# Kernel optimization log

Measured on AMD Instinct MI355X. Metric: run time of the kernel, lower is better.

The kernel has to match this reference:

```python
import jax, jax.numpy as jnp
import numpy as np

S, B, D, H, F = 1024, 8, 1024, 16, 4096
HD = D // H
EPS = 1e-5


def setup_inputs() -> dict:
    key = jax.random.key(0)
    ks = jax.random.split(key, 12)
    sc_d = 1.0 / np.sqrt(D)
    sc_f = 1.0 / np.sqrt(F)
    return {
        "src": jax.random.normal(ks[0], (S, B, D), jnp.float32),
        "in_proj_w": jax.random.uniform(ks[1], (3 * D, D), jnp.float32, -sc_d, sc_d),
        "in_proj_b": jnp.zeros((3 * D,), jnp.float32),
        "out_w": jax.random.uniform(ks[2], (D, D), jnp.float32, -sc_d, sc_d),
        "out_b": jnp.zeros((D,), jnp.float32),
        "w1": jax.random.uniform(ks[3], (F, D), jnp.float32, -sc_d, sc_d),
        "b1": jax.random.uniform(ks[4], (F,), jnp.float32, -sc_d, sc_d),
        "w2": jax.random.uniform(ks[5], (D, F), jnp.float32, -sc_f, sc_f),
        "b2": jax.random.uniform(ks[6], (D,), jnp.float32, -sc_f, sc_f),
        "g1": jnp.ones((D,), jnp.float32),
        "be1": jnp.zeros((D,), jnp.float32),
        "g2": jnp.ones((D,), jnp.float32),
        "be2": jnp.zeros((D,), jnp.float32),
    }


def _layer_norm(x, g, b):
    mu = jnp.mean(x, axis=-1, keepdims=True)
    var = jnp.mean(jnp.square(x - mu), axis=-1, keepdims=True)
    return (x - mu) * jax.lax.rsqrt(var + EPS) * g + b


def reference(src, in_proj_w, in_proj_b, out_w, out_b, w1, b1, w2, b2, g1, be1, g2, be2):
    wq, wk, wv = jnp.split(in_proj_w, 3, axis=0)
    bq, bk, bv = jnp.split(in_proj_b, 3, axis=0)
    scale = 1.0 / np.sqrt(HD)
    # src: [S, B, D] -> q/k/v: [S, B, H, HD]
    q = (src @ wq.T + bq).reshape(S, B, H, HD) * scale
    k = (src @ wk.T + bk).reshape(S, B, H, HD)
    v = (src @ wv.T + bv).reshape(S, B, H, HD)
    # full score matrix [B, H, S, S] (matches the unfused bmm/softmax/bmm)
    scores = jnp.einsum("sbhd,tbhd->bhst", q, k)
    attn = jax.nn.softmax(scores, axis=-1)
    ctx = jnp.einsum("bhst,tbhd->sbhd", attn, v).reshape(S, B, D)
    attn_out = ctx @ out_w.T + out_b
    x = _layer_norm(src + attn_out, g1, be1)
    ffn = jax.nn.relu(x @ w1.T + b1) @ w2.T + b2
    return _layer_norm(x + ffn, g2, be2)
```

## Files before the change

kernel.cpp:

```cpp
#include <hip/hip_runtime.h>
#include <hip/hip_bf16.h>
#include <stdint.h>

typedef __bf16 bf16x8 __attribute__((ext_vector_type(8)));
typedef __bf16 bf16x4 __attribute__((ext_vector_type(4)));
typedef float floatx4 __attribute__((ext_vector_type(4)));

typedef __attribute__((address_space(1))) void gvoid;
typedef __attribute__((address_space(3))) void lvoid;

__device__ __forceinline__ void async_load16(const __bf16* g, __bf16* l) {
  __builtin_amdgcn_global_load_lds((gvoid*)g, (lvoid*)l, 16, 0, 0);
}

__device__ __forceinline__ bf16x8 ld8(const float* p) {
  const floatx4 a = *(const floatx4*)p;
  const floatx4 b = *(const floatx4*)(p + 4);
  bf16x8 r;
  r[0] = (__bf16)a[0]; r[1] = (__bf16)a[1];
  r[2] = (__bf16)a[2]; r[3] = (__bf16)a[3];
  r[4] = (__bf16)b[0]; r[5] = (__bf16)b[1];
  r[6] = (__bf16)b[2]; r[7] = (__bf16)b[3];
  return r;
}

__global__ __launch_bounds__(256) void cvt_kernel(const float* __restrict__ in,
                                                  __bf16* __restrict__ out,
                                                  int n) {
  const int i = (blockIdx.x * 256 + threadIdx.x) * 8;
  if (i < n) *(bf16x8*)(out + i) = ld8(in + i);
}

constexpr int BM = 128, BN = 128, BK = 32;

template <typename AT, typename BT, int EPI>
__global__ __launch_bounds__(256, 2) void gemm_bt(
    const AT* __restrict__ A, const BT* __restrict__ Bt,
    const float* __restrict__ bias, const float* __restrict__ resf,
    const __bf16* __restrict__ resb, __bf16* __restrict__ o0,
    __bf16* __restrict__ o2, int M, int N, int K, int ldb) {
  constexpr bool AF = sizeof(AT) == 4;
  constexpr bool BF = sizeof(BT) == 4;
  __shared__ __align__(16) __bf16 As[BM * BK];
  __shared__ __align__(16) __bf16 Bs[BN * BK];
  const int tid = threadIdx.x;
  const int w = tid >> 6;
  const int lane = tid & 63;
  const int l16 = lane & 15;
  const int quad = lane >> 4;
  const int wm = (w & 1) * 64;
  const int wn = (w >> 1) * 64;
  const int bm = blockIdx.y * BM;
  const int bn = blockIdx.x * BN;

  floatx4 acc[4][4];
#pragma unroll
  for (int i = 0; i < 4; ++i)
#pragma unroll
    for (int j = 0; j < 4; ++j) acc[i][j] = (floatx4){0.f, 0.f, 0.f, 0.f};

  const int srow = tid >> 2, scol = (tid & 3) * 8;
  const int arow = lane >> 2, acol = (lane & 3) * 8;
  const AT* Ag;
  if constexpr (AF) Ag = A + (int64_t)(bm + srow) * K + scol;
  else Ag = A + (int64_t)(bm + w * 32 + arow) * K + acol;
  const BT* Bg;
  if constexpr (BF) Bg = Bt + (int64_t)(bn + srow) * ldb + scol;
  else Bg = Bt + (int64_t)(bn + w * 32 + arow) * ldb + acol;
  __bf16* AsW = As + (w * 32) * BK;
  __bf16* BsW = Bs + (w * 32) * BK;

  bf16x8 a0, a1, b0, b1;
  if constexpr (AF) {
    a0 = ld8(Ag);
    a1 = ld8(Ag + (int64_t)64 * K);
  }
  if constexpr (BF) {
    b0 = ld8(Bg);
    b1 = ld8(Bg + (int64_t)64 * ldb);
  }

  for (int k0 = 0; k0 < K; k0 += BK) {
    __syncthreads();
    if constexpr (AF) {
      *(bf16x8*)(As + tid * 8) = a0;
      *(bf16x8*)(As + 2048 + tid * 8) = a1;
    } else {
      async_load16(Ag + k0, AsW);
      async_load16(Ag + k0 + 16 * K, AsW + 16 * BK);
    }
    if constexpr (BF) {
      *(bf16x8*)(Bs + tid * 8) = b0;
      *(bf16x8*)(Bs + 2048 + tid * 8) = b1;
    } else {
      async_load16(Bg + k0, BsW);
      async_load16(Bg + k0 + 16 * ldb, BsW + 16 * BK);
    }
    __syncthreads();
    if constexpr (AF) {
      if (k0 + BK < K) {
        a0 = ld8(Ag + k0 + BK);
        a1 = ld8(Ag + k0 + BK + (int64_t)64 * K);
      }
    }
    if constexpr (BF) {
      if (k0 + BK < K) {
        b0 = ld8(Bg + k0 + BK);
        b1 = ld8(Bg + k0 + BK + (int64_t)64 * ldb);
      }
    }
    bf16x8 af[4], bfr[4];
#pragma unroll
    for (int i = 0; i < 4; ++i) {
      af[i] = *(const bf16x8*)(As + (wm + i * 16 + l16) * BK + quad * 8);
      bfr[i] = *(const bf16x8*)(Bs + (wn + i * 16 + l16) * BK + quad * 8);
    }
#pragma unroll
    for (int mi = 0; mi < 4; ++mi)
#pragma unroll
      for (int ni = 0; ni < 4; ++ni)
        acc[mi][ni] = __builtin_amdgcn_mfma_f32_16x16x32_bf16(
            af[mi], bfr[ni], acc[mi][ni], 0, 0, 0);
  }

#pragma unroll
  for (int ni = 0; ni < 4; ++ni) {
    const int gn = bn + wn + ni * 16 + l16;
    const float bv = (EPI == 3) ? 0.f : bias[gn];
#pragma unroll
    for (int mi = 0; mi < 4; ++mi) {
#pragma unroll
      for (int r = 0; r < 4; ++r) {
        const int gm = bm + wm + mi * 16 + quad * 4 + r;
        float v = acc[mi][ni][r] + bv;
        if (EPI == 0) {
          if (gn < 2048) {
            o0[(int64_t)gm * 2048 + gn] = (__bf16)(gn < 1024 ? v * 0.125f : v);
          } else {
            const int nn = gn - 2048, hh = nn >> 6, d = nn & 63;
            const int s = gm >> 3, b = gm & 7;
            o2[((b * 16 + hh) * 64 + d) * 1024 + s] = (__bf16)v;
          }
        } else {
          if (EPI == 1) v += resf[(int64_t)gm * N + gn];
          if (EPI == 3 || EPI == 4) v += (float)resb[(int64_t)gm * N + gn];
          if (EPI == 2) v = fmaxf(v, 0.f);
          o0[(int64_t)gm * N + gn] = (__bf16)v;
        }
      }
    }
  }
}

__global__ __launch_bounds__(256) void attn_flash(
    const __bf16* __restrict__ qk, const __bf16* __restrict__ vT,
    __bf16* __restrict__ ctx) {
  constexpr int S = 1024, PSTR = 36;
  constexpr int ROWSTR = 8 * 2048;
  __shared__ __align__(16) __bf16 Kb[2][2048];
  __shared__ __align__(16) __bf16 Vb[2][2048];
  __shared__ __align__(16) __bf16 Pt[4][32 * PSTR];
  const int tid = threadIdx.x;
  const int w = tid >> 6;
  const int lane = tid & 63;
  const int l16 = lane & 15;
  const int quad = lane >> 4;
  const int bh = blockIdx.y, bidx = bh >> 4, h = bh & 15;
  const int qbase = blockIdx.x * 128 + w * 32;

  const __bf16* qp =
      qk + ((int64_t)(qbase + l16) * 8 + bidx) * 2048 + h * 64 + quad * 8;
  bf16x8 aq[2][2];
  aq[0][0] = *(const bf16x8*)qp;
  aq[0][1] = *(const bf16x8*)(qp + 32);
  aq[1][0] = *(const bf16x8*)(qp + 16 * ROWSTR);
  aq[1][1] = *(const bf16x8*)(qp + 16 * ROWSTR + 32);

  const __bf16* kg = qk + 1024 +
      ((int64_t)((w >> 1) * 16 + l16) * 8 + bidx) * 2048 + h * 64 +
      ((w & 1) * 4 + quad) * 8;
  const __bf16* vg =
      vT + ((int64_t)bh * 64 + w * 16 + l16) * 1024 + quad * 8;
  __bf16* pt = Pt[w];

  floatx4 o[2][4];
  float la[2][4];
#pragma unroll
  for (int rt = 0; rt < 2; ++rt)
#pragma unroll
    for (int j = 0; j < 4; ++j) {
      o[rt][j] = (floatx4){0.f, 0.f, 0.f, 0.f};
      la[rt][j] = 0.f;
    }

  async_load16(kg, Kb[0] + w * 512);
  async_load16(vg, Vb[0] + w * 512);
  int cur = 0;

  for (int t0 = 0; t0 < S; t0 += 32) {
    __syncthreads();
    if (t0 + 32 < S) {
      async_load16(kg + (int64_t)(t0 + 32) * ROWSTR, Kb[cur ^ 1] + w * 512);
      async_load16(vg + (t0 + 32), Vb[cur ^ 1] + w * 512);
    }

    bf16x8 kf[4], vv[4];
#pragma unroll
    for (int f = 0; f < 4; ++f) {
      kf[f] = *(const bf16x8*)(Kb[cur] + f * 512 + lane * 8);
      vv[f] = *(const bf16x8*)(Vb[cur] + f * 512 + lane * 8);
    }

    floatx4 s00 = (floatx4){0.f, 0.f, 0.f, 0.f};
    floatx4 s01 = (floatx4){0.f, 0.f, 0.f, 0.f};
    floatx4 s10 = (floatx4){0.f, 0.f, 0.f, 0.f};
    floatx4 s11 = (floatx4){0.f, 0.f, 0.f, 0.f};
    s00 = __builtin_amdgcn_mfma_f32_16x16x32_bf16(aq[0][0], kf[0], s00, 0, 0, 0);
    s00 = __builtin_amdgcn_mfma_f32_16x16x32_bf16(aq[0][1], kf[1], s00, 0, 0, 0);
    s01 = __builtin_amdgcn_mfma_f32_16x16x32_bf16(aq[0][0], kf[2], s01, 0, 0, 0);
    s01 = __builtin_amdgcn_mfma_f32_16x16x32_bf16(aq[0][1], kf[3], s01, 0, 0, 0);
    s10 = __builtin_amdgcn_mfma_f32_16x16x32_bf16(aq[1][0], kf[0], s10, 0, 0, 0);
    s10 = __builtin_amdgcn_mfma_f32_16x16x32_bf16(aq[1][1], kf[1], s10, 0, 0, 0);
    s11 = __builtin_amdgcn_mfma_f32_16x16x32_bf16(aq[1][0], kf[2], s11, 0, 0, 0);
    s11 = __builtin_amdgcn_mfma_f32_16x16x32_bf16(aq[1][1], kf[3], s11, 0, 0, 0);

#pragma unroll
    for (int r = 0; r < 4; ++r) {
      const int row0 = (quad * 4 + r) * PSTR;
      const float p00 = __expf(s00[r]);
      const float p01 = __expf(s01[r]);
      la[0][r] += p00 + p01;
      pt[row0 + l16] = (__bf16)p00;
      pt[row0 + 16 + l16] = (__bf16)p01;
      const int row1 = (16 + quad * 4 + r) * PSTR;
      const float p10 = __expf(s10[r]);
      const float p11 = __expf(s11[r]);
      la[1][r] += p10 + p11;
      pt[row1 + l16] = (__bf16)p10;
      pt[row1 + 16 + l16] = (__bf16)p11;
    }
    const bf16x8 pa0 = *(const bf16x8*)(pt + l16 * PSTR + quad * 8);
    const bf16x8 pa1 = *(const bf16x8*)(pt + (16 + l16) * PSTR + quad * 8);
#pragma unroll
    for (int j = 0; j < 4; ++j) {
      o[0][j] = __builtin_amdgcn_mfma_f32_16x16x32_bf16(pa0, vv[j], o[0][j], 0, 0, 0);
      o[1][j] = __builtin_amdgcn_mfma_f32_16x16x32_bf16(pa1, vv[j], o[1][j], 0, 0, 0);
    }
    cur ^= 1;
  }

#pragma unroll
  for (int rt = 0; rt < 2; ++rt)
#pragma unroll
    for (int r = 0; r < 4; ++r) {
      float s = la[rt][r];
      s += __shfl_xor(s, 1, 64);
      s += __shfl_xor(s, 2, 64);
      s += __shfl_xor(s, 4, 64);
      s += __shfl_xor(s, 8, 64);
      la[rt][r] = s;
    }
#pragma unroll
  for (int rt = 0; rt < 2; ++rt)
#pragma unroll
    for (int j = 0; j < 4; ++j)
#pragma unroll
      for (int r = 0; r < 4; ++r) {
        const int row = qbase + rt * 16 + quad * 4 + r;
        const int gm = row * 8 + bidx;
        ctx[(int64_t)gm * 1024 + h * 64 + j * 16 + l16] =
            (__bf16)(o[rt][j][r] / la[rt][r]);
      }
}

template <typename OutT>
__global__ __launch_bounds__(256) void ln_kernel(const __bf16* __restrict__ y,
                                                 const float* __restrict__ g,
                                                 const float* __restrict__ be,
                                                 OutT* __restrict__ out) {
  constexpr int D = 1024;
  const int row = blockIdx.x;
  const int tid = threadIdx.x;
  const __bf16* yr = y + (int64_t)row * D;
  const int c0 = tid * 4;
  const bf16x4 raw = *(const bf16x4*)(yr + c0);
  float v[4];
#pragma unroll
  for (int j = 0; j < 4; ++j) v[j] = (float)raw[j];
  float s = v[0] + v[1] + v[2] + v[3];
  float sq = v[0] * v[0] + v[1] * v[1] + v[2] * v[2] + v[3] * v[3];
#pragma unroll
  for (int off = 1; off < 64; off <<= 1) {
    s += __shfl_xor(s, off, 64);
    sq += __shfl_xor(sq, off, 64);
  }
  __shared__ float ls[4], lq[4];
  const int w = tid >> 6;
  if ((tid & 63) == 0) {
    ls[w] = s;
    lq[w] = sq;
  }
  __syncthreads();
  s = ls[0] + ls[1] + ls[2] + ls[3];
  sq = lq[0] + lq[1] + lq[2] + lq[3];
  const float mean = s * (1.f / D);
  const float var = sq * (1.f / D) - mean * mean;
  const float inv = rsqrtf(var + 1e-5f);
  const floatx4 gv = *(const floatx4*)(g + c0);
  const floatx4 bv = *(const floatx4*)(be + c0);
  if constexpr (sizeof(OutT) == 4) {
    floatx4 ov;
#pragma unroll
    for (int j = 0; j < 4; ++j) ov[j] = (v[j] - mean) * inv * gv[j] + bv[j];
    *(floatx4*)((float*)out + (int64_t)row * D + c0) = ov;
  } else {
    bf16x4 ov;
#pragma unroll
    for (int j = 0; j < 4; ++j)
      ov[j] = (__bf16)((v[j] - mean) * inv * gv[j] + bv[j]);
    *(bf16x4*)((__bf16*)out + (int64_t)row * D + c0) = ov;
  }
}

extern "C" void kernel_launch(void* const* d_in, const int* in_sizes, int n_in,
                              void* d_out, int out_size, void* d_ws,
                              size_t ws_size, hipStream_t stream) {
  const float* src = (const float*)d_in[0];
  const float* in_proj_w = (const float*)d_in[1];
  const float* in_proj_b = (const float*)d_in[2];
  const float* out_w = (const float*)d_in[3];
  const float* out_b = (const float*)d_in[4];
  const float* w1 = (const float*)d_in[5];
  const float* b1 = (const float*)d_in[6];
  const float* w2 = (const float*)d_in[7];
  const float* b2 = (const float*)d_in[8];
  const float* g1 = (const float*)d_in[9];
  const float* be1 = (const float*)d_in[10];
  const float* g2 = (const float*)d_in[11];
  const float* be2 = (const float*)d_in[12];

  char* ws = (char*)d_ws;
  char* out8 = (char*)d_out;
  __bf16* qkb = (__bf16*)ws;
  __bf16* vb = (__bf16*)out8;
  __bf16* ipwb = (__bf16*)(out8 + (16ull << 20));
  __bf16* srcb = (__bf16*)(ws + (32ull << 20));
  __bf16* ctxb = (__bf16*)(out8 + (16ull << 20));
  __bf16* owb = (__bf16*)ws;
  __bf16* yb = (__bf16*)(ws + (2ull << 20));
  __bf16* xb = (__bf16*)out8;
  __bf16* w1b = (__bf16*)ws;
  __bf16* w2b = (__bf16*)(ws + (8ull << 20));
  __bf16* hb = (__bf16*)(out8 + (16ull << 20));
  __bf16* zb = (__bf16*)(ws + (16ull << 20));

  const bool big = ws_size >= ((size_t)48 << 20);

  cvt_kernel<<<1536, 256, 0, stream>>>(in_proj_w, ipwb, 3 * 1024 * 1024);
  if (big) {
    cvt_kernel<<<4096, 256, 0, stream>>>(src, srcb, 8 * 1024 * 1024);
    gemm_bt<__bf16, __bf16, 0><<<dim3(24, 64), 256, 0, stream>>>(
        srcb, ipwb, in_proj_b, nullptr, nullptr, qkb, vb, 8192, 3072, 1024,
        1024);
  } else {
    gemm_bt<float, __bf16, 0><<<dim3(24, 64), 256, 0, stream>>>(
        src, ipwb, in_proj_b, nullptr, nullptr, qkb, vb, 8192, 3072, 1024,
        1024);
  }
  attn_flash<<<dim3(8, 128), 256, 0, stream>>>(qkb, vb, ctxb);
  cvt_kernel<<<512, 256, 0, stream>>>(out_w, owb, 1024 * 1024);
  gemm_bt<__bf16, __bf16, 1><<<dim3(8, 64), 256, 0, stream>>>(
      ctxb, owb, out_b, src, nullptr, yb, nullptr, 8192, 1024, 1024, 1024);
  ln_kernel<__bf16><<<8192, 256, 0, stream>>>(yb, g1, be1, xb);
  cvt_kernel<<<2048, 256, 0, stream>>>(w1, w1b, 4 * 1024 * 1024);
  cvt_kernel<<<2048, 256, 0, stream>>>(w2, w2b, 4 * 1024 * 1024);
  for (int qd = 0; qd < 4; ++qd) {
    gemm_bt<__bf16, __bf16, 2><<<dim3(8, 64), 256, 0, stream>>>(
        xb, w1b + (int64_t)qd * 1024 * 1024, b1 + qd * 1024, nullptr, nullptr,
        hb, nullptr, 8192, 1024, 1024, 1024);
    if (qd == 0)
      gemm_bt<__bf16, __bf16, 4><<<dim3(8, 64), 256, 0, stream>>>(
          hb, w2b + qd * 1024, b2, nullptr, xb, zb, nullptr, 8192, 1024, 1024,
          4096);
    else
      gemm_bt<__bf16, __bf16, 3><<<dim3(8, 64), 256, 0, stream>>>(
          hb, w2b + qd * 1024, nullptr, nullptr, zb, zb, nullptr, 8192, 1024,
          1024, 4096);
  }
  ln_kernel<float><<<8192, 256, 0, stream>>>(zb, g2, be2, (float*)d_out);
}
```

Baseline: 626.9 us.

## Add 128x256 double-buffered 512-thread GEMM and halve FFN chunk count

Adds a new bf16 GEMM kernel with a 128x256 output tile, 8 waves, and a BK=64 k-step split into two halves. It stages tiles through double-buffered LDS with async global-to-LDS loads, swizzled addressing and raised wave priority around the MFMA block. On the large-workspace path it replaces all GEMMs with this kernel, and it processes the FFN in two 2048-wide chunks instead of four. The workspace buffers are moved to fit the larger hidden chunk. The aim is more data reuse per tile, overlap of loads with MFMA work, and fewer launches and partial-sum passes. The cost is higher LDS and register pressure, which could limit occupancy.

```diff
diff --git a/kernel.cpp b/kernel.cpp
--- a/kernel.cpp
+++ b/kernel.cpp
@@ -29,6 +29,120 @@
                                                   int n) {
   const int i = (blockIdx.x * 256 + threadIdx.x) * 8;
   if (i < n) *(bf16x8*)(out + i) = ld8(in + i);
+}
+
+template <int EPI>
+__global__ __launch_bounds__(512, 2) void gemm128(
+    const __bf16* __restrict__ A, const __bf16* __restrict__ Bt,
+    const float* __restrict__ bias, const float* __restrict__ resf,
+    const __bf16* __restrict__ resb, __bf16* __restrict__ o0,
+    __bf16* __restrict__ o2, int M, int N, int K, int ldb) {
+  __shared__ __align__(16) __bf16 AS[2][2][4096];
+  __shared__ __align__(16) __bf16 BS[2][2][8192];
+  const int tid = threadIdx.x;
+  const int w = tid >> 6;
+  const int lane = tid & 63;
+  const int l16 = lane & 15;
+  const int quad = lane >> 4;
+  const int wm = w >> 2;
+  const int wn = w & 3;
+  const int bm = blockIdx.y * 128;
+  const int bn = blockIdx.x * 256;
+  const int NT = K >> 6;
+
+  floatx4 acc[4][4];
+#pragma unroll
+  for (int i = 0; i < 4; ++i)
+#pragma unroll
+    for (int j = 0; j < 4; ++j) acc[i][j] = (floatx4){0.f, 0.f, 0.f, 0.f};
+
+  const int xfs = ((lane >> 2) & 3) ^ ((lane >> 4) & 1);
+  const int strow = w * 16 + (lane >> 2);
+  const int stcol = ((lane & 3) ^ xfs) * 8;
+  const __bf16* stA = A + (int64_t)(bm + strow) * K + stcol;
+  const __bf16* stB0 = Bt + (int64_t)(bn + strow) * ldb + stcol;
+  const __bf16* stB1 = stB0 + (int64_t)128 * ldb;
+
+  const int xq = quad ^ (l16 & 3) ^ ((l16 >> 2) & 1);
+  const int ard = (wm * 64 + l16) * 32 + xq * 8;
+  const int brd = (wn * 64 + l16) * 32 + xq * 8;
+
+  async_load16(stA, &AS[0][0][w * 512]);
+  async_load16(stB0, &BS[0][0][w * 512]);
+  async_load16(stB1, &BS[0][0][4096 + w * 512]);
+  async_load16(stA + 32, &AS[0][1][w * 512]);
+  async_load16(stB0 + 32, &BS[0][1][w * 512]);
+  async_load16(stB1 + 32, &BS[0][1][4096 + w * 512]);
+  asm volatile("s_waitcnt vmcnt(3)" ::: "memory");
+  __builtin_amdgcn_s_barrier();
+  __builtin_amdgcn_sched_barrier(0);
+
+  for (int T = 0; T < NT; ++T) {
+    const int buf = T & 1;
+#pragma unroll
+    for (int p = 0; p < 2; ++p) {
+      const int kh = p;
+      if (T + 1 < NT) {
+        const int koff = (T + 1) * 64 + kh * 32;
+        async_load16(stA + koff, &AS[buf ^ 1][kh][w * 512]);
+        async_load16(stB0 + koff, &BS[buf ^ 1][kh][w * 512]);
+        async_load16(stB1 + koff, &BS[buf ^ 1][kh][4096 + w * 512]);
+      }
+      bf16x8 af[4], bfr[4];
+#pragma unroll
+      for (int i = 0; i < 4; ++i) {
+        af[i] = *(const bf16x8*)&AS[buf][kh][ard + i * 512];
+        bfr[i] = *(const bf16x8*)&BS[buf][kh][brd + i * 512];
+      }
+      __builtin_amdgcn_sched_barrier(0);
+      __builtin_amdgcn_s_barrier();
+      asm volatile("s_waitcnt lgkmcnt(0)" ::: "memory");
+      __builtin_amdgcn_sched_barrier(0);
+      __builtin_amdgcn_s_setprio(1);
+#pragma unroll
+      for (int mi = 0; mi < 4; ++mi)
+#pragma unroll
+        for (int ni = 0; ni < 4; ++ni)
+          acc[mi][ni] = __builtin_amdgcn_mfma_f32_16x16x32_bf16(
+              af[mi], bfr[ni], acc[mi][ni], 0, 0, 0);
+      __builtin_amdgcn_s_setprio(0);
+      __builtin_amdgcn_sched_barrier(0);
+      if (p == 0 && T + 1 >= NT)
+        asm volatile("s_waitcnt vmcnt(0)" ::: "memory");
+      else
+        asm volatile("s_waitcnt vmcnt(3)" ::: "memory");
+      __builtin_amdgcn_s_barrier();
+      __builtin_amdgcn_sched_barrier(0);
+    }
+  }
+
+#pragma unroll
+  for (int ni = 0; ni < 4; ++ni) {
+    const int gn = bn + wn * 64 + ni * 16 + l16;
+    const float bv = (EPI == 3) ? 0.f : bias[gn];
+#pragma unroll
+    for (int ai = 0; ai < 4; ++ai) {
+#pragma unroll
+      for (int r = 0; r < 4; ++r) {
+        const int gm = bm + wm * 64 + ai * 16 + quad * 4 + r;
+        float v = acc[ai][ni][r] + bv;
+        if (EPI == 0) {
+          if (gn < 2048) {
+            o0[(int64_t)gm * 2048 + gn] = (__bf16)(gn < 1024 ? v * 0.125f : v);
+          } else {
+            const int nn = gn - 2048, hh = nn >> 6, d = nn & 63;
+            const int s = gm >> 3, b = gm & 7;
+            o2[((b * 16 + hh) * 64 + d) * 1024 + s] = (__bf16)v;
+          }
+        } else {
+          if (EPI == 1) v += resf[(int64_t)gm * N + gn];
+          if (EPI == 3 || EPI == 4) v += (float)resb[(int64_t)gm * N + gn];
+          if (EPI == 2) v = fmaxf(v, 0.f);
+          o0[(int64_t)gm * N + gn] = (__bf16)v;
+        }
+      }
+    }
+  }
 }
 
 constexpr int BM = 128, BN = 128, BK = 32;
@@ -349,43 +463,71 @@
   __bf16* owb = (__bf16*)ws;
   __bf16* yb = (__bf16*)(ws + (2ull << 20));
   __bf16* xb = (__bf16*)out8;
-  __bf16* w1b = (__bf16*)ws;
-  __bf16* w2b = (__bf16*)(ws + (8ull << 20));
-  __bf16* hb = (__bf16*)(out8 + (16ull << 20));
-  __bf16* zb = (__bf16*)(ws + (16ull << 20));
 
   const bool big = ws_size >= ((size_t)48 << 20);
 
-  cvt_kernel<<<1536, 256, 0, stream>>>(in_proj_w, ipwb, 3 * 1024 * 1024);
   if (big) {
+    __bf16* w1b = (__bf16*)(out8 + (16ull << 20));
+    __bf16* w2b = (__bf16*)(out8 + (24ull << 20));
+    __bf16* hb = (__bf16*)(ws + (16ull << 20));
+    __bf16* zb = (__bf16*)ws;
+
+    cvt_kernel<<<1536, 256, 0, stream>>>(in_proj_w, ipwb, 3 * 1024 * 1024);
     cvt_kernel<<<4096, 256, 0, stream>>>(src, srcb, 8 * 1024 * 1024);
-    gemm_bt<__bf16, __bf16, 0><<<dim3(24, 64), 256, 0, stream>>>(
+    gemm128<0><<<dim3(12, 64), 512, 0, stream>>>(
         srcb, ipwb, in_proj_b, nullptr, nullptr, qkb, vb, 8192, 3072, 1024,
         1024);
+    attn_flash<<<dim3(8, 128), 256, 0, stream>>>(qkb, vb, ctxb);
+    cvt_kernel<<<512, 256, 0, stream>>>(out_w, owb, 1024 * 1024);
+    gemm128<1><<<dim3(4, 64), 512, 0, stream>>>(
+        ctxb, owb, out_b, src, nullptr, yb, nullptr, 8192, 1024, 1024, 1024);
+    ln_kernel<__bf16><<<8192, 256, 0, stream>>>(yb, g1, be1, xb);
+    cvt_kernel<<<2048, 256, 0, stream>>>(w1, w1b, 4 * 1024 * 1024);
+    cvt_kernel<<<2048, 256, 0, stream>>>(w2, w2b, 4 * 1024 * 1024);
+    for (int q = 0; q < 2; ++q) {
+      gemm128<2><<<dim3(8, 64), 512, 0, stream>>>(
+          xb, w1b + (int64_t)q * 2048 * 1024, b1 + q * 2048, nullptr, nullptr,
+          hb, nullptr, 8192, 2048, 1024, 1024);
+      if (q == 0)
+        gemm128<4><<<dim3(4, 64), 512, 0, stream>>>(
+            hb, w2b + q * 2048, b2, nullptr, xb, zb, nullptr, 8192, 1024, 2048,
+            4096);
+      else
+        gemm128<3><<<dim3(4, 64), 512, 0, stream>>>(
+            hb, w2b + q * 2048, nullptr, nullptr, zb, zb, nullptr, 8192, 1024,
+            2048, 4096);
+    }
+    ln_kernel<float><<<8192, 256, 0, stream>>>(zb, g2, be2, (float*)d_out);
   } else {
+    __bf16* w1b = (__bf16*)ws;
+    __bf16* w2b = (__bf16*)(ws + (8ull << 20));
+    __bf16* hb = (__bf16*)(out8 + (16ull << 20));
+    __bf16* zb = (__bf16*)(ws + (16ull << 20));
+
+    cvt_kernel<<<1536, 256, 0, stream>>>(in_proj_w, ipwb, 3 * 1024 * 1024);
     gemm_bt<float, __bf16, 0><<<dim3(24, 64), 256, 0, stream>>>(
         src, ipwb, in_proj_b, nullptr, nullptr, qkb, vb, 8192, 3072, 1024,
         1024);
-  }
-  attn_flash<<<dim3(8, 128), 256, 0, stream>>>(qkb, vb, ctxb);
-  cvt_kernel<<<512, 256, 0, stream>>>(out_w, owb, 1024 * 1024);
-  gemm_bt<__bf16, __bf16, 1><<<dim3(8, 64), 256, 0, stream>>>(
-      ctxb, owb, out_b, src, nullptr, yb, nullptr, 8192, 1024, 1024, 1024);
-  ln_kernel<__bf16><<<8192, 256, 0, stream>>>(yb, g1, be1, xb);
-  cvt_kernel<<<2048, 256, 0, stream>>>(w1, w1b, 4 * 1024 * 1024);
-  cvt_kernel<<<2048, 256, 0, stream>>>(w2, w2b, 4 * 1024 * 1024);
-  for (int qd = 0; qd < 4; ++qd) {
-    gemm_bt<__bf16, __bf16, 2><<<dim3(8, 64), 256, 0, stream>>>(
-        xb, w1b + (int64_t)qd * 1024 * 1024, b1 + qd * 1024, nullptr, nullptr,
-        hb, nullptr, 8192, 1024, 1024, 1024);
-    if (qd == 0)
-      gemm_bt<__bf16, __bf16, 4><<<dim3(8, 64), 256, 0, stream>>>(
-          hb, w2b + qd * 1024, b2, nullptr, xb, zb, nullptr, 8192, 1024, 1024,
-          4096);
-    else
-      gemm_bt<__bf16, __bf16, 3><<<dim3(8, 64), 256, 0, stream>>>(
-          hb, w2b + qd * 1024, nullptr, nullptr, zb, zb, nullptr, 8192, 1024,
-          1024, 4096);
-  }
-  ln_kernel<float><<<8192, 256, 0, stream>>>(zb, g2, be2, (float*)d_out);
-}
+    attn_flash<<<dim3(8, 128), 256, 0, stream>>>(qkb, vb, ctxb);
+    cvt_kernel<<<512, 256, 0, stream>>>(out_w, owb, 1024 * 1024);
+    gemm_bt<__bf16, __bf16, 1><<<dim3(8, 64), 256, 0, stream>>>(
+        ctxb, owb, out_b, src, nullptr, yb, nullptr, 8192, 1024, 1024, 1024);
+    ln_kernel<__bf16><<<8192, 256, 0, stream>>>(yb, g1, be1, xb);
+    cvt_kernel<<<2048, 256, 0, stream>>>(w1, w1b, 4 * 1024 * 1024);
+    cvt_kernel<<<2048, 256, 0, stream>>>(w2, w2b, 4 * 1024 * 1024);
+    for (int qd = 0; qd < 4; ++qd) {
+      gemm_bt<__bf16, __bf16, 2><<<dim3(8, 64), 256, 0, stream>>>(
+          xb, w1b + (int64_t)qd * 1024 * 1024, b1 + qd * 1024, nullptr,
+          nullptr, hb, nullptr, 8192, 1024, 1024, 1024);
+      if (qd == 0)
+        gemm_bt<__bf16, __bf16, 4><<<dim3(8, 64), 256, 0, stream>>>(
+            hb, w2b + qd * 1024, b2, nullptr, xb, zb, nullptr, 8192, 1024,
+            1024, 4096);
+      else
+        gemm_bt<__bf16, __bf16, 3><<<dim3(8, 64), 256, 0, stream>>>(
+            hb, w2b + qd * 1024, nullptr, nullptr, zb, zb, nullptr, 8192, 1024,
+            1024, 4096);
+    }
+    ln_kernel<float><<<8192, 256, 0, stream>>>(zb, g2, be2, (float*)d_out);
+  }
+}
```

New measurement: 690.8 us. 10.2% more time.

## Double-buffer GEMM shared tiles and halve FFN chunk count with larger buffers

Applied to the files above, without the earlier changes.

The GEMM kernel now keeps two LDS buffers per operand. It issues the async global-to-LDS loads for the next K tile before computing on the current one, which leaves one barrier per iteration instead of two. On the large-workspace path, the buffers are remapped so the FFN runs in two chunks of width 2048 instead of four of width 1024, cutting launches and the read-modify-write passes over the fp32-free residual accumulator. Shared memory per block doubles, which may limit occupancy, and the buffer aliasing across d_out and the workspace must stay correct.

```diff
diff --git a/kernel.cpp b/kernel.cpp
--- a/kernel.cpp
+++ b/kernel.cpp
@@ -33,16 +33,15 @@
 
 constexpr int BM = 128, BN = 128, BK = 32;
 
-template <typename AT, typename BT, int EPI>
-__global__ __launch_bounds__(256, 2) void gemm_bt(
-    const AT* __restrict__ A, const BT* __restrict__ Bt,
+template <typename AT, int EPI>
+__global__ __launch_bounds__(256, 2) void gemm_db(
+    const AT* __restrict__ A, const __bf16* __restrict__ Bt,
     const float* __restrict__ bias, const float* __restrict__ resf,
     const __bf16* __restrict__ resb, __bf16* __restrict__ o0,
     __bf16* __restrict__ o2, int M, int N, int K, int ldb) {
   constexpr bool AF = sizeof(AT) == 4;
-  constexpr bool BF = sizeof(BT) == 4;
-  __shared__ __align__(16) __bf16 As[BM * BK];
-  __shared__ __align__(16) __bf16 Bs[BN * BK];
+  __shared__ __align__(16) __bf16 As[2][BM * BK];
+  __shared__ __align__(16) __bf16 Bs[2][BN * BK];
   const int tid = threadIdx.x;
   const int w = tid >> 6;
   const int lane = tid & 63;
@@ -64,56 +63,55 @@
   const AT* Ag;
   if constexpr (AF) Ag = A + (int64_t)(bm + srow) * K + scol;
   else Ag = A + (int64_t)(bm + w * 32 + arow) * K + acol;
-  const BT* Bg;
-  if constexpr (BF) Bg = Bt + (int64_t)(bn + srow) * ldb + scol;
-  else Bg = Bt + (int64_t)(bn + w * 32 + arow) * ldb + acol;
-  __bf16* AsW = As + (w * 32) * BK;
-  __bf16* BsW = Bs + (w * 32) * BK;
-
-  bf16x8 a0, a1, b0, b1;
+  const __bf16* Bg = Bt + (int64_t)(bn + w * 32 + arow) * ldb + acol;
+
+  bf16x8 a0, a1;
   if constexpr (AF) {
     a0 = ld8(Ag);
     a1 = ld8(Ag + (int64_t)64 * K);
-  }
-  if constexpr (BF) {
-    b0 = ld8(Bg);
-    b1 = ld8(Bg + (int64_t)64 * ldb);
-  }
-
+    *(bf16x8*)(As[0] + tid * 8) = a0;
+    *(bf16x8*)(As[0] + 2048 + tid * 8) = a1;
+    if (BK < K) {
+      a0 = ld8(Ag + BK);
+      a1 = ld8(Ag + BK + (int64_t)64 * K);
+    }
+  } else {
+    __bf16* AsW = As[0] + (w * 32) * BK;
+    async_load16(Ag, AsW);
+    async_load16(Ag + 16 * K, AsW + 16 * BK);
+  }
+  {
+    __bf16* BsW = Bs[0] + (w * 32) * BK;
+    async_load16(Bg, BsW);
+    async_load16(Bg + 16 * ldb, BsW + 16 * BK);
+  }
+  __syncthreads();
+
+  int cur = 0;
   for (int k0 = 0; k0 < K; k0 += BK) {
-    __syncthreads();
-    if constexpr (AF) {
-      *(bf16x8*)(As + tid * 8) = a0;
-      *(bf16x8*)(As + 2048 + tid * 8) = a1;
-    } else {
-      async_load16(Ag + k0, AsW);
-      async_load16(Ag + k0 + 16 * K, AsW + 16 * BK);
-    }
-    if constexpr (BF) {
-      *(bf16x8*)(Bs + tid * 8) = b0;
-      *(bf16x8*)(Bs + 2048 + tid * 8) = b1;
-    } else {
-      async_load16(Bg + k0, BsW);
-      async_load16(Bg + k0 + 16 * ldb, BsW + 16 * BK);
-    }
-    __syncthreads();
-    if constexpr (AF) {
-      if (k0 + BK < K) {
-        a0 = ld8(Ag + k0 + BK);
-        a1 = ld8(Ag + k0 + BK + (int64_t)64 * K);
+    const bool more = (k0 + BK) < K;
+    if (more) {
+      if constexpr (AF) {
+        *(bf16x8*)(As[cur ^ 1] + tid * 8) = a0;
+        *(bf16x8*)(As[cur ^ 1] + 2048 + tid * 8) = a1;
+        if (k0 + 2 * BK < K) {
+          a0 = ld8(Ag + k0 + 2 * BK);
+          a1 = ld8(Ag + k0 + 2 * BK + (int64_t)64 * K);
+        }
+      } else {
+        __bf16* AsW = As[cur ^ 1] + (w * 32) * BK;
+        async_load16(Ag + k0 + BK, AsW);
+        async_load16(Ag + k0 + BK + 16 * K, AsW + 16 * BK);
       }
-    }
-    if constexpr (BF) {
-      if (k0 + BK < K) {
-        b0 = ld8(Bg + k0 + BK);
-        b1 = ld8(Bg + k0 + BK + (int64_t)64 * ldb);
-      }
+      __bf16* BsW = Bs[cur ^ 1] + (w * 32) * BK;
+      async_load16(Bg + k0 + BK, BsW);
+      async_load16(Bg + k0 + BK + 16 * ldb, BsW + 16 * BK);
     }
     bf16x8 af[4], bfr[4];
 #pragma unroll
     for (int i = 0; i < 4; ++i) {
-      af[i] = *(const bf16x8*)(As + (wm + i * 16 + l16) * BK + quad * 8);
-      bfr[i] = *(const bf16x8*)(Bs + (wn + i * 16 + l16) * BK + quad * 8);
+      af[i] = *(const bf16x8*)(As[cur] + (wm + i * 16 + l16) * BK + quad * 8);
+      bfr[i] = *(const bf16x8*)(Bs[cur] + (wn + i * 16 + l16) * BK + quad * 8);
     }
 #pragma unroll
     for (int mi = 0; mi < 4; ++mi)
@@ -121,6 +119,8 @@
       for (int ni = 0; ni < 4; ++ni)
         acc[mi][ni] = __builtin_amdgcn_mfma_f32_16x16x32_bf16(
             af[mi], bfr[ni], acc[mi][ni], 0, 0, 0);
+    __syncthreads();
+    cur ^= 1;
   }
 
 #pragma unroll
@@ -349,43 +349,71 @@
   __bf16* owb = (__bf16*)ws;
   __bf16* yb = (__bf16*)(ws + (2ull << 20));
   __bf16* xb = (__bf16*)out8;
-  __bf16* w1b = (__bf16*)ws;
-  __bf16* w2b = (__bf16*)(ws + (8ull << 20));
-  __bf16* hb = (__bf16*)(out8 + (16ull << 20));
-  __bf16* zb = (__bf16*)(ws + (16ull << 20));
 
   const bool big = ws_size >= ((size_t)48 << 20);
 
-  cvt_kernel<<<1536, 256, 0, stream>>>(in_proj_w, ipwb, 3 * 1024 * 1024);
   if (big) {
+    __bf16* w1b = (__bf16*)(out8 + (16ull << 20));
+    __bf16* w2b = (__bf16*)(out8 + (24ull << 20));
+    __bf16* hb = (__bf16*)(ws + (16ull << 20));
+    __bf16* zb = (__bf16*)ws;
+
+    cvt_kernel<<<1536, 256, 0, stream>>>(in_proj_w, ipwb, 3 * 1024 * 1024);
     cvt_kernel<<<4096, 256, 0, stream>>>(src, srcb, 8 * 1024 * 1024);
-    gemm_bt<__bf16, __bf16, 0><<<dim3(24, 64), 256, 0, stream>>>(
+    gemm_db<__bf16, 0><<<dim3(24, 64), 256, 0, stream>>>(
         srcb, ipwb, in_proj_b, nullptr, nullptr, qkb, vb, 8192, 3072, 1024,
         1024);
+    attn_flash<<<dim3(8, 128), 256, 0, stream>>>(qkb, vb, ctxb);
+    cvt_kernel<<<512, 256, 0, stream>>>(out_w, owb, 1024 * 1024);
+    gemm_db<__bf16, 1><<<dim3(8, 64), 256, 0, stream>>>(
+        ctxb, owb, out_b, src, nullptr, yb, nullptr, 8192, 1024, 1024, 1024);
+    ln_kernel<__bf16><<<8192, 256, 0, stream>>>(yb, g1, be1, xb);
+    cvt_kernel<<<2048, 256, 0, stream>>>(w1, w1b, 4 * 1024 * 1024);
+    cvt_kernel<<<2048, 256, 0, stream>>>(w2, w2b, 4 * 1024 * 1024);
+    for (int q = 0; q < 2; ++q) {
+      gemm_db<__bf16, 2><<<dim3(16, 64), 256, 0, stream>>>(
+          xb, w1b + (int64_t)q * 2048 * 1024, b1 + q * 2048, nullptr, nullptr,
+          hb, nullptr, 8192, 2048, 1024, 1024);
+      if (q == 0)
+        gemm_db<__bf16, 4><<<dim3(8, 64), 256, 0, stream>>>(
+            hb, w2b + q * 2048, b2, nullptr, xb, zb, nullptr, 8192, 1024, 2048,
+            4096);
+      else
+        gemm_db<__bf16, 3><<<dim3(8, 64), 256, 0, stream>>>(
+            hb, w2b + q * 2048, nullptr, nullptr, zb, zb, nullptr, 8192, 1024,
+            2048, 4096);
+    }
+    ln_kernel<float><<<8192, 256, 0, stream>>>(zb, g2, be2, (float*)d_out);
   } else {
-    gemm_bt<float, __bf16, 0><<<dim3(24, 64), 256, 0, stream>>>(
+    __bf16* w1b = (__bf16*)ws;
+    __bf16* w2b = (__bf16*)(ws + (8ull << 20));
+    __bf16* hb = (__bf16*)(out8 + (16ull << 20));
+    __bf16* zb = (__bf16*)(ws + (16ull << 20));
+
+    cvt_kernel<<<1536, 256, 0, stream>>>(in_proj_w, ipwb, 3 * 1024 * 1024);
+    gemm_db<float, 0><<<dim3(24, 64), 256, 0, stream>>>(
         src, ipwb, in_proj_b, nullptr, nullptr, qkb, vb, 8192, 3072, 1024,
         1024);
-  }
-  attn_flash<<<dim3(8, 128), 256, 0, stream>>>(qkb, vb, ctxb);
-  cvt_kernel<<<512, 256, 0, stream>>>(out_w, owb, 1024 * 1024);
-  gemm_bt<__bf16, __bf16, 1><<<dim3(8, 64), 256, 0, stream>>>(
-      ctxb, owb, out_b, src, nullptr, yb, nullptr, 8192, 1024, 1024, 1024);
-  ln_kernel<__bf16><<<8192, 256, 0, stream>>>(yb, g1, be1, xb);
-  cvt_kernel<<<2048, 256, 0, stream>>>(w1, w1b, 4 * 1024 * 1024);
-  cvt_kernel<<<2048, 256, 0, stream>>>(w2, w2b, 4 * 1024 * 1024);
-  for (int qd = 0; qd < 4; ++qd) {
-    gemm_bt<__bf16, __bf16, 2><<<dim3(8, 64), 256, 0, stream>>>(
-        xb, w1b + (int64_t)qd * 1024 * 1024, b1 + qd * 1024, nullptr, nullptr,
-        hb, nullptr, 8192, 1024, 1024, 1024);
-    if (qd == 0)
-      gemm_bt<__bf16, __bf16, 4><<<dim3(8, 64), 256, 0, stream>>>(
-          hb, w2b + qd * 1024, b2, nullptr, xb, zb, nullptr, 8192, 1024, 1024,
-          4096);
-    else
-      gemm_bt<__bf16, __bf16, 3><<<dim3(8, 64), 256, 0, stream>>>(
-          hb, w2b + qd * 1024, nullptr, nullptr, zb, zb, nullptr, 8192, 1024,
-          1024, 4096);
-  }
-  ln_kernel<float><<<8192, 256, 0, stream>>>(zb, g2, be2, (float*)d_out);
-}
+    attn_flash<<<dim3(8, 128), 256, 0, stream>>>(qkb, vb, ctxb);
+    cvt_kernel<<<512, 256, 0, stream>>>(out_w, owb, 1024 * 1024);
+    gemm_db<__bf16, 1><<<dim3(8, 64), 256, 0, stream>>>(
+        ctxb, owb, out_b, src, nullptr, yb, nullptr, 8192, 1024, 1024, 1024);
+    ln_kernel<__bf16><<<8192, 256, 0, stream>>>(yb, g1, be1, xb);
+    cvt_kernel<<<2048, 256, 0, stream>>>(w1, w1b, 4 * 1024 * 1024);
+    cvt_kernel<<<2048, 256, 0, stream>>>(w2, w2b, 4 * 1024 * 1024);
+    for (int qd = 0; qd < 4; ++qd) {
+      gemm_db<__bf16, 2><<<dim3(8, 64), 256, 0, stream>>>(
+          xb, w1b + (int64_t)qd * 1024 * 1024, b1 + qd * 1024, nullptr,
+          nullptr, hb, nullptr, 8192, 1024, 1024, 1024);
+      if (qd == 0)
+        gemm_db<__bf16, 4><<<dim3(8, 64), 256, 0, stream>>>(
+            hb, w2b + qd * 1024, b2, nullptr, xb, zb, nullptr, 8192, 1024,
+            1024, 4096);
+      else
+        gemm_db<__bf16, 3><<<dim3(8, 64), 256, 0, stream>>>(
+            hb, w2b + qd * 1024, nullptr, nullptr, zb, zb, nullptr, 8192, 1024,
+            1024, 4096);
+    }
+    ln_kernel<float><<<8192, 256, 0, stream>>>(zb, g2, be2, (float*)d_out);
+  }
+}
```

After: 570.1 us. -9.1%, faster.
